# Kernel optimization log

Measured on AMD Instinct MI355X. Metric: run time of the kernel, lower is better.

Reference implementation:

```python
import jax, jax.numpy as jnp
import numpy as np

MARGIN = 0.3
BIG = 1e30  # finite sentinel for masked max/min (avoids inf-inf NaNs)


def setup_inputs() -> dict:
    key = jax.random.key(0)
    k1, k2 = jax.random.split(key)
    N, D = 8192, 128
    embeddings = jax.random.normal(k1, (N, D), dtype=jnp.float32)
    labels = jax.random.randint(k2, (N,), 0, 1024, dtype=jnp.int64)
    return {"embeddings": embeddings, "labels": labels}


def _pairwise_euclidean(x):
    # torch.cdist(x, x, p=2): sqrt of clamped squared distances,
    # with a double-where so sqrt(0) has no NaN gradient.
    sq = jnp.sum(x * x, axis=1)                      # [N]
    d2 = sq[:, None] + sq[None, :] - 2.0 * (x @ x.T)  # [N, N]
    d2 = jnp.maximum(d2, 0.0)
    safe = jnp.where(d2 > 0.0, d2, 1.0)
    return jnp.where(d2 > 0.0, jnp.sqrt(safe), 0.0)


def reference(embeddings, labels):
    dist = _pairwise_euclidean(embeddings)           # [N, N]
    same = labels[:, None] == labels[None, :]        # [N, N]
    eye = jnp.eye(labels.shape[0], dtype=bool)
    mask_pos = same & ~eye
    mask_neg = ~same

    hardest_pos = jnp.max(jnp.where(mask_pos, dist, -BIG), axis=1)  # [N]
    hardest_neg = jnp.min(jnp.where(mask_neg, dist, BIG), axis=1)   # [N]

    valid = jnp.any(mask_pos, axis=1) & jnp.any(mask_neg, axis=1)
    per_row = jax.nn.relu(hardest_pos - hardest_neg + MARGIN)
    per_row = jnp.where(valid, per_row, 0.0)
    cnt = jnp.sum(valid.astype(jnp.float32))
    # torch code returns 0.0 when no valid anchors
    return jnp.where(cnt > 0, jnp.sum(per_row) / jnp.maximum(cnt, 1.0), 0.0)
```

## Files before the change

### kernel.cpp

```cpp
#include <hip/hip_runtime.h>
#include <hip/hip_bf16.h>

#define NSPLIT 16
#define BIGF 1e30f
#define MARGIN 0.3f
#define DK 128

typedef __attribute__((ext_vector_type(8))) short bf16x8;
typedef __attribute__((ext_vector_type(4))) float f32x4;

#define WS_HIST 0
#define WS_GSUM 1024
#define WS_GCNT 1025
#define WS_BCNT 1026
#define WS_HP   1028
#define WS_HN   (WS_HP + 8192)
#define WS_SQ   (WS_HN + 8192)
#define WS_XB   (WS_SQ + 8192)
#define WS_ZERO_BYTES (1028 * 4)


__global__ __launch_bounds__(256) void prep_kernel(
    const float* __restrict__ x, ushort* __restrict__ xs,
    float* __restrict__ sq, unsigned* __restrict__ hist,
    const int* __restrict__ lab,
    unsigned* __restrict__ hp_bits, unsigned* __restrict__ hn_comp, int N)
{
    __shared__ float part[32][17];
    const int tid = threadIdx.x;
    const int rbase = blockIdx.x * 32;
    const int rlq = tid & 15;
    const int kc  = tid >> 4;
    bf16x8* outv = (bf16x8*)(xs + (size_t)rbase * DK);

    #pragma unroll
    for (int g = 0; g < 2; ++g) {
        int row = rbase + g * 16 + rlq;
        const float4* p = (const float4*)(x + (size_t)row * DK + kc * 8);
        float4 u = p[0], v = p[1];
        float f[8] = {u.x, u.y, u.z, u.w, v.x, v.y, v.z, v.w};
        union { bf16x8 v8; ushort us[8]; } o;
        float ps = 0.0f;
        #pragma unroll
        for (int e = 0; e < 8; ++e) {
            __hip_bfloat16 b = __float2bfloat16(f[e]);
            o.us[e] = *(ushort*)&b;
            ps += f[e] * f[e];
        }
        outv[g * 256 + tid] = o.v8;
        part[g * 16 + rlq][kc] = ps;
    }
    __syncthreads();
    if (tid < 32) {
        float s = 0.0f;
        #pragma unroll
        for (int k = 0; k < 16; ++k) s += part[tid][k];
        int row = rbase + tid;
        sq[row] = s;
        hp_bits[row] = 0u;
        hn_comp[row] = 0u;
        atomicAdd(&hist[lab[row]], 1u);
    }
}


#define ZERO_ACC(ACC)                                                     \
    _Pragma("unroll")                                                     \
    for (int mt = 0; mt < 4; ++mt)                                        \
        _Pragma("unroll")                                                 \
        for (int j = 0; j < 2; ++j)                                       \
            ACC[mt][j] = (f32x4){0.f, 0.f, 0.f, 0.f};

#define MFMA_HALF(ACC, B)                                                 \
    _Pragma("unroll")                                                     \
    for (int s = 0; s < 4; ++s) {                                         \
        bf16x8 afr[4];                                                    \
        _Pragma("unroll")                                                 \
        for (int mt = 0; mt < 4; ++mt)                                    \
            afr[mt] = *(const bf16x8*)(a_base + mt * 2048 + s * 512);     \
        _Pragma("unroll")                                                 \
        for (int mt = 0; mt < 4; ++mt)                                    \
            _Pragma("unroll")                                             \
            for (int j = 0; j < 2; ++j)                                   \
                ACC[mt][j] = __builtin_amdgcn_mfma_f32_16x16x32_bf16(     \
                    afr[mt], B[j][s], ACC[mt][j], 0, 0, 0);               \
    }

#define EPI_HALF(ACC, SQB, LB)                                            \
    _Pragma("unroll")                                                     \
    for (int mt = 0; mt < 4; ++mt) {                                      \
        int4 rl4 = *(const int4*)&laba_s[wrow + mt * 16 + quad * 4];      \
        const int rla[4] = {rl4.x, rl4.y, rl4.z, rl4.w};                  \
        _Pragma("unroll")                                                 \
        for (int r = 0; r < 4; ++r) {                                     \
            float t0 = fmaf(-2.0f, ACC[mt][0][r], SQB[0]);                \
            float t1 = fmaf(-2.0f, ACC[mt][1][r], SQB[1]);                \
            bool s0 = (rla[r] == LB[0]);                                  \
            bool s1 = (rla[r] == LB[1]);                                  \
            float cp0 = s0 ? t0 : -BIGF;                                  \
            float cp1 = s1 ? t1 : -BIGF;                                  \
            runhp[mt][r] = fmaxf(fmaxf(runhp[mt][r], cp0), cp1);          \
            float cn0 = s0 ? BIGF : t0;                                   \
            float cn1 = s1 ? BIGF : t1;                                   \
            runhn[mt][r] = fminf(fminf(runhn[mt][r], cn0), cn1);          \
        }                                                                 \
    }

__global__ __launch_bounds__(256, 2) void tile_kernel(
    const ushort* __restrict__ xs, const float* __restrict__ sq,
    const int* __restrict__ lab,
    unsigned* __restrict__ hp_bits, unsigned* __restrict__ hn_comp, int N)
{
    __shared__ ushort a_s[128 * DK];
    __shared__ int   laba_s[128];
    __shared__ float red_hp[128][2];
    __shared__ float red_hn[128][2];

    const int tid  = threadIdx.x;
    const int lane = tid & 63;
    const int wave = tid >> 6;
    const int m16  = lane & 15;
    const int quad = lane >> 4;
    const int rbase = blockIdx.x * 128;
    const int wrow = (wave >> 1) * 64;
    const int wcol = (wave & 1) * 64;

    {
        const bf16x8* srcv = (const bf16x8*)(xs + (size_t)rbase * DK);
        bf16x8* dstv = (bf16x8*)a_s;
        #pragma unroll
        for (int i = 0; i < 8; ++i)
            dstv[tid + i * 256] = srcv[tid + i * 256];
    }
    if (tid < 128) laba_s[tid] = lab[rbase + tid];
    __syncthreads();

    float runhp[4][4], runhn[4][4];
    #pragma unroll
    for (int mt = 0; mt < 4; ++mt)
        #pragma unroll
        for (int r = 0; r < 4; ++r) { runhp[mt][r] = -BIGF; runhn[mt][r] = BIGF; }

    const ushort* a_base = a_s + wrow * DK + quad * 128 + m16 * 8;

    const int cols_per_split = N / NSPLIT;
    const int cbegin = blockIdx.y * cols_per_split + wcol;

    unsigned voff[4];
    #pragma unroll
    for (int c = 0; c < 4; ++c)
        voff[c] = (unsigned)(cbegin + c * 16) * DK + quad * 128 + m16 * 8;

    #pragma unroll 1
    for (int ci = 0; ci < cols_per_split; ci += 128) {
        bf16x8 b0[2][4];
        #pragma unroll
        for (int j = 0; j < 2; ++j)
            #pragma unroll
            for (int s = 0; s < 4; ++s)
                b0[j][s] = *(const bf16x8*)(xs + voff[j] + s * 512);
        float sqb0[2]; int lb0[2];
        #pragma unroll
        for (int j = 0; j < 2; ++j) {
            int colg = cbegin + ci + j * 16 + m16;
            sqb0[j] = sq[colg]; lb0[j] = lab[colg];
        }

        f32x4 acc[4][2];
        ZERO_ACC(acc);
        MFMA_HALF(acc, b0);

        bf16x8 b1[2][4];
        #pragma unroll
        for (int j = 0; j < 2; ++j)
            #pragma unroll
            for (int s = 0; s < 4; ++s)
                b1[j][s] = *(const bf16x8*)(xs + voff[2 + j] + s * 512);
        float sqb1[2]; int lb1[2];
        #pragma unroll
        for (int j = 0; j < 2; ++j) {
            int colg = cbegin + ci + (2 + j) * 16 + m16;
            sqb1[j] = sq[colg]; lb1[j] = lab[colg];
        }

        EPI_HALF(acc, sqb0, lb0);

        ZERO_ACC(acc);
        MFMA_HALF(acc, b1);
        EPI_HALF(acc, sqb1, lb1);

        #pragma unroll
        for (int c = 0; c < 4; ++c) voff[c] += 128 * DK;
    }

    #pragma unroll
    for (int mt = 0; mt < 4; ++mt)
        #pragma unroll
        for (int r = 0; r < 4; ++r) {
            #pragma unroll
            for (int o = 8; o > 0; o >>= 1) {
                runhp[mt][r] = fmaxf(runhp[mt][r], __shfl_xor(runhp[mt][r], o, 16));
                runhn[mt][r] = fminf(runhn[mt][r], __shfl_xor(runhn[mt][r], o, 16));
            }
        }

    if (m16 == 0) {
        #pragma unroll
        for (int mt = 0; mt < 4; ++mt)
            #pragma unroll
            for (int r = 0; r < 4; ++r) {
                int rowl = wrow + mt * 16 + quad * 4 + r;
                red_hp[rowl][wave & 1] = runhp[mt][r];
                red_hn[rowl][wave & 1] = runhn[mt][r];
            }
    }
    __syncthreads();
    if (tid < 128) {
        float thp = fmaxf(red_hp[tid][0], red_hp[tid][1]);
        float thn = fminf(red_hn[tid][0], red_hn[tid][1]);
        float sqa = sq[rbase + tid];
        float d2p = fmaxf(sqa + thp, 0.0f);
        float d2n = fmaxf(sqa + thn, 0.0f);
        atomicMax(&hp_bits[rbase + tid], __float_as_uint(d2p));
        atomicMax(&hn_comp[rbase + tid], ~__float_as_uint(d2n));
    }
}

__global__ void finalize_kernel(const unsigned* __restrict__ hp_bits,
                                const unsigned* __restrict__ hn_comp,
                                const int* __restrict__ lab,
                                const unsigned* __restrict__ hist,
                                float* __restrict__ gsum, float* __restrict__ gcnt,
                                unsigned* __restrict__ bcount,
                                float* __restrict__ out, int N)
{
    __shared__ float s_sum[256];
    __shared__ float s_cnt[256];
    int tid = threadIdx.x;
    int row = blockIdx.x * 256 + tid;
    float loss = 0.0f, cv = 0.0f;
    if (row < N) {
        unsigned c = hist[lab[row]];
        bool valid = (c >= 2u) && (c < (unsigned)N);
        if (valid) {
            float dp = sqrtf(__uint_as_float(hp_bits[row]));
            float dn = sqrtf(__uint_as_float(~hn_comp[row]));
            loss = fmaxf(dp - dn + MARGIN, 0.0f);
            cv = 1.0f;
        }
    }
    s_sum[tid] = loss; s_cnt[tid] = cv;
    __syncthreads();
    for (int o = 128; o > 0; o >>= 1) {
        if (tid < o) { s_sum[tid] += s_sum[tid + o]; s_cnt[tid] += s_cnt[tid + o]; }
        __syncthreads();
    }
    if (tid == 0) {
        atomicAdd(gsum, s_sum[0]);
        atomicAdd(gcnt, s_cnt[0]);
        __threadfence();
        unsigned old = atomicAdd(bcount, 1u);
        if (old == gridDim.x - 1) {
            float s = atomicAdd(gsum, 0.0f);
            float c = atomicAdd(gcnt, 0.0f);
            out[0] = (c > 0.0f) ? s / c : 0.0f;
        }
    }
}

extern "C" void kernel_launch(void* const* d_in, const int* in_sizes, int n_in,
                              void* d_out, int out_size, void* d_ws, size_t ws_size,
                              hipStream_t stream) {
    const float* x = (const float*)d_in[0];
    const int* lab = (const int*)d_in[1];
    float* out = (float*)d_out;
    const int N = in_sizes[1];

    unsigned* ws = (unsigned*)d_ws;
    unsigned* hist    = ws + WS_HIST;
    float* gsum = (float*)(ws + WS_GSUM);
    float* gcnt = (float*)(ws + WS_GCNT);
    unsigned* bcount = ws + WS_BCNT;
    unsigned* hp_bits = ws + WS_HP;
    unsigned* hn_comp = ws + WS_HN;
    float* sq = (float*)(ws + WS_SQ);
    ushort* xs = (ushort*)(ws + WS_XB);

    hipMemsetAsync(d_ws, 0, (size_t)WS_ZERO_BYTES, stream);
    prep_kernel<<<N / 32, 256, 0, stream>>>(x, xs, sq, hist, lab, hp_bits, hn_comp, N);
    dim3 grid(N / 128, NSPLIT);
    tile_kernel<<<grid, 256, 0, stream>>>(xs, sq, lab, hp_bits, hn_comp, N);
    finalize_kernel<<<N / 256, 256, 0, stream>>>(hp_bits, hn_comp, lab, hist,
                                                 gsum, gcnt, bcount, out, N);
}
```

Baseline: 97.35 us.

## Software-pipeline B-fragment loads across halves and shuffle-reduce row norms in prep

The tile loop now prefetches the next half-tile of B fragments, norms and labels while the current MFMA and epilogue run, and issues the first load before the initial barrier. This is meant to hide global-load latency behind compute. The accumulator zeroing is folded into the first MFMA step. The prep kernel replaces its shared-memory partial-sum reduction and barrier with a 16-lane shuffle reduction and uses a different thread-to-row mapping, which changes the bf16 store pattern. The extra prefetched fragments raise register pressure, which could hurt at two blocks per SM.

```diff
diff --git a/kernel.cpp b/kernel.cpp
--- a/kernel.cpp
+++ b/kernel.cpp
@@ -26,16 +26,14 @@
     const int* __restrict__ lab,
     unsigned* __restrict__ hp_bits, unsigned* __restrict__ hn_comp, int N)
 {
-    __shared__ float part[32][17];
     const int tid = threadIdx.x;
     const int rbase = blockIdx.x * 32;
-    const int rlq = tid & 15;
-    const int kc  = tid >> 4;
-    bf16x8* outv = (bf16x8*)(xs + (size_t)rbase * DK);
+    const int rl = tid >> 4;
+    const int kc = tid & 15;
 
     #pragma unroll
     for (int g = 0; g < 2; ++g) {
-        int row = rbase + g * 16 + rlq;
+        int row = rbase + g * 16 + rl;
         const float4* p = (const float4*)(x + (size_t)row * DK + kc * 8);
         float4 u = p[0], v = p[1];
         float f[8] = {u.x, u.y, u.z, u.w, v.x, v.y, v.z, v.w};
@@ -47,31 +45,20 @@
             o.us[e] = *(ushort*)&b;
             ps += f[e] * f[e];
         }
-        outv[g * 256 + tid] = o.v8;
-        part[g * 16 + rlq][kc] = ps;
-    }
-    __syncthreads();
-    if (tid < 32) {
-        float s = 0.0f;
-        #pragma unroll
-        for (int k = 0; k < 16; ++k) s += part[tid][k];
-        int row = rbase + tid;
-        sq[row] = s;
-        hp_bits[row] = 0u;
-        hn_comp[row] = 0u;
-        atomicAdd(&hist[lab[row]], 1u);
-    }
-}
-
-
-#define ZERO_ACC(ACC)                                                     \
-    _Pragma("unroll")                                                     \
-    for (int mt = 0; mt < 4; ++mt)                                        \
-        _Pragma("unroll")                                                 \
-        for (int j = 0; j < 2; ++j)                                       \
-            ACC[mt][j] = (f32x4){0.f, 0.f, 0.f, 0.f};
-
-#define MFMA_HALF(ACC, B)                                                 \
+        ((bf16x8*)xs)[(size_t)(row >> 4) * 256 + kc * 16 + rl] = o.v8;
+        #pragma unroll
+        for (int o2 = 8; o2 > 0; o2 >>= 1) ps += __shfl_xor(ps, o2, 16);
+        if (kc == 0) {
+            sq[row] = ps;
+            hp_bits[row] = 0u;
+            hn_comp[row] = 0u;
+            atomicAdd(&hist[lab[row]], 1u);
+        }
+    }
+}
+
+
+#define MFMA_HALF_INIT(ACC, B)                                            \
     _Pragma("unroll")                                                     \
     for (int s = 0; s < 4; ++s) {                                         \
         bf16x8 afr[4];                                                    \
@@ -83,7 +70,9 @@
             _Pragma("unroll")                                             \
             for (int j = 0; j < 2; ++j)                                   \
                 ACC[mt][j] = __builtin_amdgcn_mfma_f32_16x16x32_bf16(     \
-                    afr[mt], B[j][s], ACC[mt][j], 0, 0, 0);               \
+                    afr[mt], B[j][s],                                     \
+                    (s == 0) ? (f32x4){0.f, 0.f, 0.f, 0.f} : ACC[mt][j],  \
+                    0, 0, 0);                                             \
     }
 
 #define EPI_HALF(ACC, SQB, LB)                                            \
@@ -106,6 +95,18 @@
         }                                                                 \
     }
 
+#define LOAD_HALF(B, SQB, LB, CHUNK0, CIN)                                \
+    _Pragma("unroll")                                                     \
+    for (int j = 0; j < 2; ++j) {                                         \
+        _Pragma("unroll")                                                 \
+        for (int s = 0; s < 4; ++s)                                       \
+            B[j][s] = *(const bf16x8*)(xs + voff0                         \
+                       + (unsigned)(CIN) * DK + (CHUNK0 + j) * 2048       \
+                       + s * 512);                                        \
+        int colg = cbegin + (CIN) + (CHUNK0 + j) * 16 + m16;              \
+        SQB[j] = sq[colg];  LB[j] = lab[colg];                            \
+    }
+
 __global__ __launch_bounds__(256, 2) void tile_kernel(
     const ushort* __restrict__ xs, const float* __restrict__ sq,
     const int* __restrict__ lab,
@@ -133,6 +134,15 @@
             dstv[tid + i * 256] = srcv[tid + i * 256];
     }
     if (tid < 128) laba_s[tid] = lab[rbase + tid];
+
+    const int cols_per_split = N / NSPLIT;
+    const int cbegin = blockIdx.y * cols_per_split + wcol;
+    const unsigned voff0 = (unsigned)cbegin * DK + quad * 128 + m16 * 8;
+
+    bf16x8 b0[2][4], b1[2][4];
+    float sqb0[2], sqb1[2]; int lb0[2], lb1[2];
+    LOAD_HALF(b0, sqb0, lb0, 0, 0);
+
     __syncthreads();
 
     float runhp[4][4], runhn[4][4];
@@ -143,54 +153,20 @@
 
     const ushort* a_base = a_s + wrow * DK + quad * 128 + m16 * 8;
 
-    const int cols_per_split = N / NSPLIT;
-    const int cbegin = blockIdx.y * cols_per_split + wcol;
-
-    unsigned voff[4];
-    #pragma unroll
-    for (int c = 0; c < 4; ++c)
-        voff[c] = (unsigned)(cbegin + c * 16) * DK + quad * 128 + m16 * 8;
-
     #pragma unroll 1
     for (int ci = 0; ci < cols_per_split; ci += 128) {
-        bf16x8 b0[2][4];
-        #pragma unroll
-        for (int j = 0; j < 2; ++j)
-            #pragma unroll
-            for (int s = 0; s < 4; ++s)
-                b0[j][s] = *(const bf16x8*)(xs + voff[j] + s * 512);
-        float sqb0[2]; int lb0[2];
-        #pragma unroll
-        for (int j = 0; j < 2; ++j) {
-            int colg = cbegin + ci + j * 16 + m16;
-            sqb0[j] = sq[colg]; lb0[j] = lab[colg];
-        }
-
         f32x4 acc[4][2];
-        ZERO_ACC(acc);
-        MFMA_HALF(acc, b0);
-
-        bf16x8 b1[2][4];
-        #pragma unroll
-        for (int j = 0; j < 2; ++j)
-            #pragma unroll
-            for (int s = 0; s < 4; ++s)
-                b1[j][s] = *(const bf16x8*)(xs + voff[2 + j] + s * 512);
-        float sqb1[2]; int lb1[2];
-        #pragma unroll
-        for (int j = 0; j < 2; ++j) {
-            int colg = cbegin + ci + (2 + j) * 16 + m16;
-            sqb1[j] = sq[colg]; lb1[j] = lab[colg];
-        }
-
+
+        MFMA_HALF_INIT(acc, b0);
+        LOAD_HALF(b1, sqb1, lb1, 2, ci);
         EPI_HALF(acc, sqb0, lb0);
 
-        ZERO_ACC(acc);
-        MFMA_HALF(acc, b1);
+        MFMA_HALF_INIT(acc, b1);
+        {
+            int cin = (ci + 128 < cols_per_split) ? (ci + 128) : ci;
+            LOAD_HALF(b0, sqb0, lb0, 0, cin);
+        }
         EPI_HALF(acc, sqb1, lb1);
-
-        #pragma unroll
-        for (int c = 0; c < 4; ++c) voff[c] += 128 * DK;
     }
 
     #pragma unroll
```

New measurement: 92.97 us. -4.5%, faster.
